# Optimization experiments

Hardware: AMD Instinct MI355X
Metric: run time of the kernel (lower is better)

The kernel has to match this reference:

```python
import jax, jax.numpy as jnp
import numpy as np
from math import sqrt

B, H, S, D = 4, 16, 8192, 64
M = 64  # num_samples (<= D since ortho_features=True)
SCALE = 0.1  # keep exp() numerically sane for randn inputs


def _gram_schmidt(mat):
    # unnormalized Gram-Schmidt over columns, matching the torch module
    d, m = mat.shape
    out = np.zeros_like(mat)
    out[:, 0] = mat[:, 0]
    for i in range(1, m):
        v = mat[:, i]
        U = out[:, :i]                      # [d, i]
        coef = (U.T @ v) / np.sum(U * U, axis=0)
        out[:, i] = v - U @ coef
    return out


def setup_inputs() -> dict:
    key = jax.random.key(0)
    kq, kk, kv = jax.random.split(key, 3)
    query = jax.random.normal(kq, (B, H, S, D), dtype=jnp.float32) * SCALE
    key_t = jax.random.normal(kk, (B, H, S, D), dtype=jnp.float32) * SCALE
    value = jax.random.normal(kv, (B, H, S, D), dtype=jnp.float32) * SCALE
    rng = np.random.default_rng(0)
    omega = jnp.asarray(_gram_schmidt(rng.standard_normal((D, M)).astype(np.float32)))
    return {"query": query, "key": key_t, "value": value, "omega": omega}


def _pos_features(x, omega, m):
    # 1/sqrt(m) * exp(-||x||^2/2) * exp(x @ omega)   -> [..., S, m]
    h = jnp.exp(-0.5 * jnp.sum(x * x, axis=-1)) * (1.0 / sqrt(m))  # [B,H,S]
    return h[..., None] * jnp.exp(jnp.einsum('bhsd,dm->bhsm', x, omega))


def reference(query, key, value, omega):
    d = query.shape[-1]
    m = omega.shape[-1]
    q_prime = _pos_features(query, omega, m)   # [B,H,S,m]
    k_prime = _pos_features(key, omega, m)     # [B,H,S,m]
    ones = jnp.ones(value.shape[:-1] + (1,), dtype=value.dtype)
    C = jnp.concatenate([value, ones], axis=-1)               # [B,H,S,d+1]
    buf1 = jnp.einsum('bhsm,bhsc->bhmc', k_prime, C)          # [B,H,m,d+1]
    buf2 = jnp.einsum('bhsm,bhmc->bhsc', q_prime, buf1)       # [B,H,S,d+1]
    num = buf2[..., :d]                                       # [B,H,S,d]
    den = buf2[..., d:]                                       # [B,H,S,1]
    return num / den
```

## Files before the change

kernel.cpp:

```cpp
#include <hip/hip_runtime.h>

typedef short short8 __attribute__((ext_vector_type(8)));
typedef short s4b __attribute__((ext_vector_type(4)));
typedef float f32x4 __attribute__((ext_vector_type(4)));

namespace {
constexpr int Sc = 8192, Dc = 64;
constexpr int NH = 64;
constexpr int CROWS = 256;
constexpr int SLABS = CROWS / 16;
constexpr int NCH1 = Sc / CROWS;
constexpr int PSTRIDE = 4160;
constexpr int CH2 = 1024;
constexpr int TPT2 = CH2 / 64;
constexpr int NCHUNK2 = Sc / CH2;
}

__device__ __forceinline__ unsigned bf16rtne(float x) {
  unsigned u = __builtin_bit_cast(unsigned, x);
  return (u + 0x7fffu + ((u >> 16) & 1u)) >> 16;
}
__device__ __forceinline__ void bsplitu(float x, unsigned& hi, unsigned& lo) {
  unsigned u = __builtin_bit_cast(unsigned, x);
  unsigned rh = (u + 0x7fffu + ((u >> 16) & 1u)) & 0xffff0000u;
  hi = rh >> 16;
  float res = x - __builtin_bit_cast(float, rh);
  lo = __builtin_bit_cast(unsigned, res) >> 16;
}
__device__ __forceinline__ unsigned pkhl(float x) {
  unsigned u = __builtin_bit_cast(unsigned, x);
  unsigned rh = (u + 0x7fffu + ((u >> 16) & 1u)) & 0xffff0000u;
  float res = x - __builtin_bit_cast(float, rh);
  return (rh >> 16) | (__builtin_bit_cast(unsigned, res) & 0xffff0000u);
}
__device__ __forceinline__ void bsplit(float x, short& hi, short& lo) {
  unsigned p = pkhl(x);
  hi = (short)(p & 0xffff);
  lo = (short)(p >> 16);
}
__device__ __forceinline__ short8 exhi(uint4 q0, uint4 q1) {
  union { unsigned u[4]; short8 s; } r;
  r.u[0] = __builtin_amdgcn_perm(q0.y, q0.x, 0x05040100u);
  r.u[1] = __builtin_amdgcn_perm(q0.w, q0.z, 0x05040100u);
  r.u[2] = __builtin_amdgcn_perm(q1.y, q1.x, 0x05040100u);
  r.u[3] = __builtin_amdgcn_perm(q1.w, q1.z, 0x05040100u);
  return r.s;
}
__device__ __forceinline__ short8 exlo(uint4 q0, uint4 q1) {
  union { unsigned u[4]; short8 s; } r;
  r.u[0] = __builtin_amdgcn_perm(q0.y, q0.x, 0x07060302u);
  r.u[1] = __builtin_amdgcn_perm(q0.w, q0.z, 0x07060302u);
  r.u[2] = __builtin_amdgcn_perm(q1.y, q1.x, 0x07060302u);
  r.u[3] = __builtin_amdgcn_perm(q1.w, q1.z, 0x07060302u);
  return r.s;
}
__device__ __forceinline__ f32x4 mfma16(s4b a, s4b b, f32x4 c) {
#if __has_builtin(__builtin_amdgcn_mfma_f32_16x16x16bf16_1k)
  return __builtin_amdgcn_mfma_f32_16x16x16bf16_1k(a, b, c, 0, 0, 0);
#else
  f32x4 d;
  asm("v_mfma_f32_16x16x16_bf16 %0, %1, %2, %3" : "=v"(d) : "v"(a), "v"(b), "v"(c));
  return d;
#endif
}

__global__ void p0(const float* __restrict__ omega, short* __restrict__ wT) {
  int i = blockIdx.x * 256 + threadIdx.x;
  if (i < 4096) {
    int m = i >> 6, d = i & 63;
    short hi, lo;
    bsplit(omega[d * 64 + m], hi, lo);
    wT[m * 64 + d] = hi;
    wT[4096 + m * 64 + d] = lo;
  }
}

__global__ __launch_bounds__(256, 2) void p1(
    const float* __restrict__ Kg, const float* __restrict__ Vg,
    const short* __restrict__ wT, float* __restrict__ part) {
  const int t = threadIdx.x;
  const int lane = t & 63;
  const int w = t >> 6;
  const int a = lane & 15;
  const int g = lane >> 4;
  const int wid = blockIdx.x * 4 + w;
  const int bh = wid >> 5;
  const int ci = wid & 31;
  const float* Kb = Kg + ((size_t)bh * Sc + (size_t)ci * CROWS) * Dc;
  const float* Vb = Vg + ((size_t)bh * Sc + (size_t)ci * CROWS) * Dc;

  short8 wfh[4][2], wfl[4][2];
#pragma unroll
  for (int mt = 0; mt < 4; ++mt)
#pragma unroll
    for (int ks = 0; ks < 2; ++ks) {
      int off = (16 * mt + a) * 64 + 32 * ks + 8 * g;
      wfh[mt][ks] = *(const short8*)(wT + off);
      wfl[mt][ks] = *(const short8*)(wT + 4096 + off);
    }

  f32x4 acc[4][4];
#pragma unroll
  for (int mt = 0; mt < 4; ++mt)
#pragma unroll
    for (int ct = 0; ct < 4; ++ct) acc[mt][ct] = (f32x4){0.f, 0.f, 0.f, 0.f};
  float den[4] = {0.f, 0.f, 0.f, 0.f};

  float4 kf[4];
  float vf[16];
  auto loadK = [&](int sl) {
    const float* kb = Kb + ((size_t)sl * 16 + a) * 64 + 8 * g;
    kf[0] = *(const float4*)(kb);
    kf[1] = *(const float4*)(kb + 4);
    kf[2] = *(const float4*)(kb + 32);
    kf[3] = *(const float4*)(kb + 36);
  };
  auto loadV = [&](int sl) {
    const float* vb = Vb + ((size_t)sl * 16 + 4 * g) * 64 + a;
#pragma unroll
    for (int ct = 0; ct < 4; ++ct)
#pragma unroll
      for (int j = 0; j < 4; ++j) vf[ct * 4 + j] = vb[j * 64 + 16 * ct];
  };

  loadK(0);
  loadV(0);

  for (int sl = 0; sl < SLABS; ++sl) {
    float ps = kf[0].x * kf[0].x + kf[0].y * kf[0].y + kf[0].z * kf[0].z + kf[0].w * kf[0].w;
    ps += kf[1].x * kf[1].x + kf[1].y * kf[1].y + kf[1].z * kf[1].z + kf[1].w * kf[1].w;
    ps += kf[2].x * kf[2].x + kf[2].y * kf[2].y + kf[2].z * kf[2].z + kf[2].w * kf[2].w;
    ps += kf[3].x * kf[3].x + kf[3].y * kf[3].y + kf[3].z * kf[3].z + kf[3].w * kf[3].w;
    ps += __shfl_xor(ps, 16, 64);
    ps += __shfl_xor(ps, 32, 64);

    short8 ah[2], al[2];
#pragma unroll
    for (int ks = 0; ks < 2; ++ks) {
      float v[8] = {kf[2 * ks].x, kf[2 * ks].y, kf[2 * ks].z, kf[2 * ks].w,
                    kf[2 * ks + 1].x, kf[2 * ks + 1].y, kf[2 * ks + 1].z, kf[2 * ks + 1].w};
#pragma unroll
      for (int i = 0; i < 8; ++i) {
        unsigned h, l;
        bsplitu(v[i], h, l);
        ah[ks][i] = (short)h;
        al[ks][i] = (short)l;
      }
    }
    if (sl + 1 < SLABS) loadK(sl + 1);

    f32x4 X[4];
#pragma unroll
    for (int mt = 0; mt < 4; ++mt) X[mt] = (f32x4){0.f, 0.f, 0.f, 0.f};
#pragma unroll
    for (int ks = 0; ks < 2; ++ks)
#pragma unroll
      for (int mt = 0; mt < 4; ++mt) {
        X[mt] = __builtin_amdgcn_mfma_f32_16x16x32_bf16(ah[ks], wfh[mt][ks], X[mt], 0, 0, 0);
        X[mt] = __builtin_amdgcn_mfma_f32_16x16x32_bf16(ah[ks], wfl[mt][ks], X[mt], 0, 0, 0);
        X[mt] = __builtin_amdgcn_mfma_f32_16x16x32_bf16(al[ks], wfh[mt][ks], X[mt], 0, 0, 0);
      }

    float sq[4];
#pragma unroll
    for (int r = 0; r < 4; ++r) sq[r] = __shfl(ps, 20 * g + r, 64);

    s4b PA[4];
#pragma unroll
    for (int mt = 0; mt < 4; ++mt) {
#pragma unroll
      for (int r = 0; r < 4; ++r) {
        float p_ = 0.125f * __expf(X[mt][r] - 0.5f * sq[r]);
        den[mt] += p_;
        PA[mt][r] = (short)bf16rtne(p_);
      }
    }

    s4b VB[4];
#pragma unroll
    for (int ct = 0; ct < 4; ++ct)
#pragma unroll
      for (int j = 0; j < 4; ++j) VB[ct][j] = (short)bf16rtne(vf[ct * 4 + j]);
    if (sl + 1 < SLABS) loadV(sl + 1);

#pragma unroll
    for (int mt = 0; mt < 4; ++mt)
#pragma unroll
      for (int ct = 0; ct < 4; ++ct) acc[mt][ct] = mfma16(PA[mt], VB[ct], acc[mt][ct]);
  }

  float* pp = part + (size_t)wid * PSTRIDE;
#pragma unroll
  for (int mt = 0; mt < 4; ++mt)
#pragma unroll
    for (int ct = 0; ct < 4; ++ct)
#pragma unroll
      for (int r = 0; r < 4; ++r)
        pp[(16 * mt + 4 * g + r) * 64 + 16 * ct + a] = acc[mt][ct][r];
#pragma unroll
  for (int mt = 0; mt < 4; ++mt) {
    float v = den[mt];
    v += __shfl_xor(v, 16, 64);
    v += __shfl_xor(v, 32, 64);
    if (g == 0) pp[4096 + 16 * mt + a] = v;
  }
}

__global__ __launch_bounds__(256) void p1r(
    const float* __restrict__ part, float* __restrict__ b1,
    float* __restrict__ den) {
  int o = blockIdx.x * 256 + threadIdx.x;
  if (o >= NH * PSTRIDE) return;
  int bh = o / PSTRIDE, i = o % PSTRIDE;
  const float* p = part + (size_t)bh * NCH1 * PSTRIDE + i;
  float s = 0.f;
#pragma unroll
  for (int c = 0; c < NCH1; ++c) s += p[(size_t)c * PSTRIDE];
  if (i < 4096) b1[bh * 4096 + i] = s;
  else den[bh * 64 + (i - 4096)] = s;
}

__global__ __launch_bounds__(256, 2) void p2(
    const float* __restrict__ Qg, const short* __restrict__ wT,
    const float* __restrict__ b1, const float* __restrict__ den,
    float* __restrict__ out) {
  __shared__ unsigned Qpk[64 * 68];
  __shared__ unsigned QP[64 * 68];
  __shared__ short B1h[64 * 72], B1l[64 * 72];
  __shared__ float denv[64];
  __shared__ float ssq[64];

  const int t = threadIdx.x;
  const int lane = t & 63;
  const int w = t >> 6;
  const int a = lane & 15;
  const int g = lane >> 4;
  const int bh = blockIdx.x / NCHUNK2, ch = blockIdx.x % NCHUNK2;
  const float* Qb = Qg + ((size_t)bh * Sc + (size_t)ch * CH2) * Dc;

  short8 wfh[4][2], wfl[4][2];
#pragma unroll
  for (int mt = 0; mt < 4; ++mt)
#pragma unroll
    for (int ks = 0; ks < 2; ++ks) {
      int off = (a + 16 * mt) * 64 + 32 * ks + 8 * g;
      wfh[mt][ks] = *(const short8*)(wT + off);
      wfl[mt][ks] = *(const short8*)(wT + 4096 + off);
    }

  const float* b1g = b1 + (size_t)bh * 4096;
  for (int i = t; i < 4096; i += 256) {
    int m = i >> 6, c = i & 63;
    short hi, lo;
    bsplit(b1g[i], hi, lo);
    B1h[c * 72 + m] = hi;
    B1l[c * 72 + m] = lo;
  }
  if (t < 64) denv[t] = den[bh * 64 + t];

  float4 qreg[4];
  auto load_tile = [&](int tile) {
    const float4* Qt = (const float4*)(Qb + (size_t)tile * 64 * Dc);
#pragma unroll
    for (int rr = 0; rr < 4; ++rr) qreg[rr] = Qt[rr * 256 + t];
  };
  auto store_tile = [&]() {
#pragma unroll
    for (int rr = 0; rr < 4; ++rr) {
      int idx = rr * 256 + t;
      int row = idx >> 4;
      int c4 = idx & 15;
      float4 kv = qreg[rr];
      uint4 qp;
      qp.x = pkhl(kv.x); qp.y = pkhl(kv.y);
      qp.z = pkhl(kv.z); qp.w = pkhl(kv.w);
      *(uint4*)&Qpk[row * 68 + 4 * c4] = qp;
      float ps = kv.x * kv.x + kv.y * kv.y + kv.z * kv.z + kv.w * kv.w;
      ps += __shfl_xor(ps, 1, 64); ps += __shfl_xor(ps, 2, 64);
      ps += __shfl_xor(ps, 4, 64); ps += __shfl_xor(ps, 8, 64);
      if (c4 == 0) ssq[row] = ps;
    }
  };

  load_tile(0);
  store_tile();
  __syncthreads();

  for (int tile = 0; tile < TPT2; ++tile) {
    if (tile + 1 < TPT2) load_tile(tile + 1);

    f32x4 X[4];
#pragma unroll
    for (int mt = 0; mt < 4; ++mt) X[mt] = (f32x4){0.f, 0.f, 0.f, 0.f};
#pragma unroll
    for (int ks = 0; ks < 2; ++ks) {
      const unsigned* qb = &Qpk[(16 * w + a) * 68 + 32 * ks + 8 * g];
      uint4 q0 = *(const uint4*)qb;
      uint4 q1 = *(const uint4*)(qb + 4);
      short8 ah = exhi(q0, q1), al = exlo(q0, q1);
#pragma unroll
      for (int mt = 0; mt < 4; ++mt) {
        X[mt] = __builtin_amdgcn_mfma_f32_16x16x32_bf16(ah, wfh[mt][ks], X[mt], 0, 0, 0);
        X[mt] = __builtin_amdgcn_mfma_f32_16x16x32_bf16(ah, wfl[mt][ks], X[mt], 0, 0, 0);
        X[mt] = __builtin_amdgcn_mfma_f32_16x16x32_bf16(al, wfh[mt][ks], X[mt], 0, 0, 0);
      }
    }

    float sq[4];
#pragma unroll
    for (int r = 0; r < 4; ++r) sq[r] = ssq[16 * w + 4 * g + r];
    float dv[4];
#pragma unroll
    for (int mt = 0; mt < 4; ++mt) dv[mt] = denv[16 * mt + a];
    float dn[4] = {0.f, 0.f, 0.f, 0.f};
#pragma unroll
    for (int mt = 0; mt < 4; ++mt) {
#pragma unroll
      for (int r = 0; r < 4; ++r) {
        float p_ = 0.125f * __expf(X[mt][r] - 0.5f * sq[r]);
        dn[r] = fmaf(p_, dv[mt], dn[r]);
        QP[(16 * w + 4 * g + r) * 68 + 16 * mt + a] = pkhl(p_);
      }
    }
#pragma unroll
    for (int r = 0; r < 4; ++r) {
      dn[r] += __shfl_xor(dn[r], 1, 64);
      dn[r] += __shfl_xor(dn[r], 2, 64);
      dn[r] += __shfl_xor(dn[r], 4, 64);
      dn[r] += __shfl_xor(dn[r], 8, 64);
    }
    __syncthreads();

    f32x4 O[4];
#pragma unroll
    for (int ct = 0; ct < 4; ++ct) O[ct] = (f32x4){0.f, 0.f, 0.f, 0.f};
#pragma unroll
    for (int ks = 0; ks < 2; ++ks) {
      const unsigned* qb = &QP[(16 * w + a) * 68 + 32 * ks + 8 * g];
      uint4 r0 = *(const uint4*)qb;
      uint4 r1 = *(const uint4*)(qb + 4);
      short8 qh = exhi(r0, r1), ql = exlo(r0, r1);
#pragma unroll
      for (int ct = 0; ct < 4; ++ct) {
        short8 bh_ = *(const short8*)&B1h[(16 * ct + a) * 72 + 32 * ks + 8 * g];
        short8 bl_ = *(const short8*)&B1l[(16 * ct + a) * 72 + 32 * ks + 8 * g];
        O[ct] = __builtin_amdgcn_mfma_f32_16x16x32_bf16(qh, bh_, O[ct], 0, 0, 0);
        O[ct] = __builtin_amdgcn_mfma_f32_16x16x32_bf16(qh, bl_, O[ct], 0, 0, 0);
        O[ct] = __builtin_amdgcn_mfma_f32_16x16x32_bf16(ql, bh_, O[ct], 0, 0, 0);
      }
    }

    float inv[4];
#pragma unroll
    for (int r = 0; r < 4; ++r) inv[r] = 1.0f / dn[r];
    float* ob = out + ((size_t)bh * Sc + (size_t)ch * CH2 + tile * 64 + 16 * w + 4 * g) * 64;
#pragma unroll
    for (int ct = 0; ct < 4; ++ct)
#pragma unroll
      for (int r = 0; r < 4; ++r)
        ob[r * 64 + 16 * ct + a] = O[ct][r] * inv[r];
    __syncthreads();
    if (tile + 1 < TPT2) store_tile();
    __syncthreads();
  }
}

extern "C" void kernel_launch(void* const* d_in, const int* in_sizes, int n_in,
                              void* d_out, int out_size, void* d_ws, size_t ws_size,
                              hipStream_t stream) {
  const float* Q = (const float*)d_in[0];
  const float* K = (const float*)d_in[1];
  const float* V = (const float*)d_in[2];
  const float* omega = (const float*)d_in[3];
  float* outp = (float*)d_out;
  float* part = (float*)d_out;
  float* b1 = (float*)d_ws;
  float* den = b1 + (size_t)NH * 4096;
  short* wT = (short*)(den + NH * 64);

  p0<<<16, 256, 0, stream>>>(omega, wT);
  p1<<<NH * NCH1 / 4, 256, 0, stream>>>(K, V, wT, part);
  p1r<<<(NH * PSTRIDE + 255) / 256, 256, 0, stream>>>(part, b1, den);
  p2<<<NH * NCHUNK2, 256, 0, stream>>>(Q, wT, b1, den, outp);
}
```

Before: 156.8 us.

## Drop split-bf16 K projection, halve chunk rows, and reduce partials in LDS

After: 189.7 us. 21.0% more time.

```diff
diff --git a/kernel.cpp b/kernel.cpp
--- a/kernel.cpp
+++ b/kernel.cpp
@@ -7,10 +7,10 @@
 namespace {
 constexpr int Sc = 8192, Dc = 64;
 constexpr int NH = 64;
-constexpr int CROWS = 256;
+constexpr int CROWS = 128;
 constexpr int SLABS = CROWS / 16;
-constexpr int NCH1 = Sc / CROWS;
 constexpr int PSTRIDE = 4160;
+constexpr int PCHUNK = 16;
 constexpr int CH2 = 1024;
 constexpr int TPT2 = CH2 / 64;
 constexpr int NCHUNK2 = Sc / CH2;
@@ -19,13 +19,6 @@
 __device__ __forceinline__ unsigned bf16rtne(float x) {
   unsigned u = __builtin_bit_cast(unsigned, x);
   return (u + 0x7fffu + ((u >> 16) & 1u)) >> 16;
-}
-__device__ __forceinline__ void bsplitu(float x, unsigned& hi, unsigned& lo) {
-  unsigned u = __builtin_bit_cast(unsigned, x);
-  unsigned rh = (u + 0x7fffu + ((u >> 16) & 1u)) & 0xffff0000u;
-  hi = rh >> 16;
-  float res = x - __builtin_bit_cast(float, rh);
-  lo = __builtin_bit_cast(unsigned, res) >> 16;
 }
 __device__ __forceinline__ unsigned pkhl(float x) {
   unsigned u = __builtin_bit_cast(unsigned, x);
@@ -75,36 +68,35 @@
   }
 }
 
-__global__ __launch_bounds__(256, 2) void p1(
+__global__ __launch_bounds__(256, 4) void p1(
     const float* __restrict__ Kg, const float* __restrict__ Vg,
     const short* __restrict__ wT, float* __restrict__ part) {
+  __shared__ float red[2 * PSTRIDE];
+
   const int t = threadIdx.x;
   const int lane = t & 63;
   const int w = t >> 6;
   const int a = lane & 15;
   const int g = lane >> 4;
-  const int wid = blockIdx.x * 4 + w;
-  const int bh = wid >> 5;
-  const int ci = wid & 31;
-  const float* Kb = Kg + ((size_t)bh * Sc + (size_t)ci * CROWS) * Dc;
-  const float* Vb = Vg + ((size_t)bh * Sc + (size_t)ci * CROWS) * Dc;
-
-  short8 wfh[4][2], wfl[4][2];
+  const int h = blockIdx.x >> 4;
+  const int cb = blockIdx.x & 15;
+  const int ci = cb * 4 + w;
+  const float* Kb = Kg + ((size_t)h * Sc + (size_t)ci * CROWS) * Dc;
+  const float* Vb = Vg + ((size_t)h * Sc + (size_t)ci * CROWS) * Dc;
+
+  short8 wfh[4][2];
 #pragma unroll
   for (int mt = 0; mt < 4; ++mt)
 #pragma unroll
-    for (int ks = 0; ks < 2; ++ks) {
-      int off = (16 * mt + a) * 64 + 32 * ks + 8 * g;
-      wfh[mt][ks] = *(const short8*)(wT + off);
-      wfl[mt][ks] = *(const short8*)(wT + 4096 + off);
-    }
+    for (int ks = 0; ks < 2; ++ks)
+      wfh[mt][ks] = *(const short8*)(wT + (16 * mt + a) * 64 + 32 * ks + 8 * g);
 
   f32x4 acc[4][4];
 #pragma unroll
   for (int mt = 0; mt < 4; ++mt)
 #pragma unroll
     for (int ct = 0; ct < 4; ++ct) acc[mt][ct] = (f32x4){0.f, 0.f, 0.f, 0.f};
-  float den[4] = {0.f, 0.f, 0.f, 0.f};
+  float dpart[4] = {0.f, 0.f, 0.f, 0.f};
 
   float4 kf[4];
   float vf[16];
@@ -134,18 +126,13 @@
     ps += __shfl_xor(ps, 16, 64);
     ps += __shfl_xor(ps, 32, 64);
 
-    short8 ah[2], al[2];
+    short8 ah[2];
 #pragma unroll
     for (int ks = 0; ks < 2; ++ks) {
       float v[8] = {kf[2 * ks].x, kf[2 * ks].y, kf[2 * ks].z, kf[2 * ks].w,
                     kf[2 * ks + 1].x, kf[2 * ks + 1].y, kf[2 * ks + 1].z, kf[2 * ks + 1].w};
 #pragma unroll
-      for (int i = 0; i < 8; ++i) {
-        unsigned h, l;
-        bsplitu(v[i], h, l);
-        ah[ks][i] = (short)h;
-        al[ks][i] = (short)l;
-      }
+      for (int i = 0; i < 8; ++i) ah[ks][i] = (short)bf16rtne(v[i]);
     }
     if (sl + 1 < SLABS) loadK(sl + 1);
 
@@ -155,11 +142,8 @@
 #pragma unroll
     for (int ks = 0; ks < 2; ++ks)
 #pragma unroll
-      for (int mt = 0; mt < 4; ++mt) {
+      for (int mt = 0; mt < 4; ++mt)
         X[mt] = __builtin_amdgcn_mfma_f32_16x16x32_bf16(ah[ks], wfh[mt][ks], X[mt], 0, 0, 0);
-        X[mt] = __builtin_amdgcn_mfma_f32_16x16x32_bf16(ah[ks], wfl[mt][ks], X[mt], 0, 0, 0);
-        X[mt] = __builtin_amdgcn_mfma_f32_16x16x32_bf16(al[ks], wfh[mt][ks], X[mt], 0, 0, 0);
-      }
 
     float sq[4];
 #pragma unroll
@@ -171,7 +155,7 @@
 #pragma unroll
       for (int r = 0; r < 4; ++r) {
         float p_ = 0.125f * __expf(X[mt][r] - 0.5f * sq[r]);
-        den[mt] += p_;
+        dpart[mt] += p_;
         PA[mt][r] = (short)bf16rtne(p_);
       }
     }
@@ -189,21 +173,46 @@
       for (int ct = 0; ct < 4; ++ct) acc[mt][ct] = mfma16(PA[mt], VB[ct], acc[mt][ct]);
   }
 
-  float* pp = part + (size_t)wid * PSTRIDE;
-#pragma unroll
-  for (int mt = 0; mt < 4; ++mt)
-#pragma unroll
-    for (int ct = 0; ct < 4; ++ct)
-#pragma unroll
-      for (int r = 0; r < 4; ++r)
-        pp[(16 * mt + 4 * g + r) * 64 + 16 * ct + a] = acc[mt][ct][r];
+  float dv[4];
 #pragma unroll
   for (int mt = 0; mt < 4; ++mt) {
-    float v = den[mt];
+    float v = dpart[mt];
     v += __shfl_xor(v, 16, 64);
     v += __shfl_xor(v, 32, 64);
-    if (g == 0) pp[4096 + 16 * mt + a] = v;
-  }
+    dv[mt] = v;
+  }
+  if (w < 2) {
+    float* rb = red + w * PSTRIDE;
+#pragma unroll
+    for (int mt = 0; mt < 4; ++mt)
+#pragma unroll
+      for (int ct = 0; ct < 4; ++ct)
+#pragma unroll
+        for (int r = 0; r < 4; ++r)
+          rb[(16 * mt + 4 * g + r) * 64 + 16 * ct + a] = acc[mt][ct][r];
+    if (g == 0) {
+#pragma unroll
+      for (int mt = 0; mt < 4; ++mt) rb[4096 + 16 * mt + a] = dv[mt];
+    }
+  }
+  __syncthreads();
+  if (w >= 2) {
+    float* rb = red + (w - 2) * PSTRIDE;
+#pragma unroll
+    for (int mt = 0; mt < 4; ++mt)
+#pragma unroll
+      for (int ct = 0; ct < 4; ++ct)
+#pragma unroll
+        for (int r = 0; r < 4; ++r)
+          rb[(16 * mt + 4 * g + r) * 64 + 16 * ct + a] += acc[mt][ct][r];
+    if (g == 0) {
+#pragma unroll
+      for (int mt = 0; mt < 4; ++mt) rb[4096 + 16 * mt + a] += dv[mt];
+    }
+  }
+  __syncthreads();
+  float* pp = part + (size_t)blockIdx.x * PSTRIDE;
+  for (int i = t; i < PSTRIDE; i += 256) pp[i] = red[i] + red[PSTRIDE + i];
 }
 
 __global__ __launch_bounds__(256) void p1r(
@@ -212,10 +221,10 @@
   int o = blockIdx.x * 256 + threadIdx.x;
   if (o >= NH * PSTRIDE) return;
   int bh = o / PSTRIDE, i = o % PSTRIDE;
-  const float* p = part + (size_t)bh * NCH1 * PSTRIDE + i;
+  const float* p = part + (size_t)bh * PCHUNK * PSTRIDE + i;
   float s = 0.f;
 #pragma unroll
-  for (int c = 0; c < NCH1; ++c) s += p[(size_t)c * PSTRIDE];
+  for (int c = 0; c < PCHUNK; ++c) s += p[(size_t)c * PSTRIDE];
   if (i < 4096) b1[bh * 4096 + i] = s;
   else den[bh * 64 + (i - 4096)] = s;
 }
@@ -379,7 +388,7 @@
   short* wT = (short*)(den + NH * 64);
 
   p0<<<16, 256, 0, stream>>>(omega, wT);
-  p1<<<NH * NCH1 / 4, 256, 0, stream>>>(K, V, wT, part);
+  p1<<<NH * PCHUNK, 256, 0, stream>>>(K, V, wT, part);
   p1r<<<(NH * PSTRIDE + 255) / 256, 256, 0, stream>>>(part, b1, den);
   p2<<<NH * NCHUNK2, 256, 0, stream>>>(Q, wT, b1, den, outp);
 }
```
